# Kernel optimization log

Hardware: AMD Instinct MI355X
Metric: run time of the kernel (lower is better)

Reference implementation:

```python
import jax, jax.numpy as jnp
import numpy as np

EPS = 1e-12  # torch F.normalize eps

def _l2norm(x):
    n = jnp.linalg.norm(x, axis=-1, keepdims=True)
    return x / jnp.maximum(n, EPS)

def _encode(h, mask, W, b):
    # h: [B,S,H], mask: [B,S] int
    h = h * mask[..., None].astype(h.dtype)      # zero padded tokens
    pooled = h[:, 0]                             # pooling_type='cls'
    col = h[:, 1:] @ W + b                       # colbert_linear on tokens 1:
    return _l2norm(pooled), _l2norm(col)         # normalize=True


def setup_inputs() -> dict:
    key = jax.random.key(0)
    k1, k2, k3, k4, k5, k6 = jax.random.split(key, 6)
    Q, Sq, C, Sc, H, D = 64, 32, 256, 256, 768, 128
    return {
        "q_hidden": jax.random.normal(k1, (Q, Sq, H), jnp.float32),
        "c_hidden": jax.random.normal(k2, (C, Sc, H), jnp.float32),
        "W": jax.random.normal(k3, (H, D), jnp.float32) / np.sqrt(H).astype(np.float32),
        "b": jax.random.normal(k4, (D,), jnp.float32) * 0.01,
        "q_mask": jax.random.randint(k5, (Q, Sq), 0, 2, jnp.int32),
        "c_mask": jax.random.randint(k6, (C, Sc), 0, 2, jnp.int32),
    }


def reference(q_hidden, c_hidden, W, b, q_mask, c_mask):
    q_pooled, q_col = _encode(q_hidden, q_mask, W, b)   # q_col: [Q, Sq-1, D]
    c_pooled, c_col = _encode(c_hidden, c_mask, W, b)   # c_col: [C, Sc-1, D]
    # MaxSim late interaction (get_batch_colbert_sim)
    token_sim = jnp.einsum('qin,cjn->qicj', q_col, c_col)  # [Q, Sq-1, C, Sc-1]
    sim = token_sim.max(axis=-1)                           # max over doc tokens j
    denom = q_mask[:, 1:].sum(-1, keepdims=True).astype(sim.dtype)
    sim = sim.sum(axis=1) / denom                          # [Q, C]
    return sim, q_pooled, c_pooled
```

## Files before the change

kernel.cpp:

```cpp
#include <hip/hip_runtime.h>
#include <hip/hip_bf16.h>

#define QN 64
#define SQ 32
#define CN 256
#define SC 256
#define HD 768
#define DD 128

typedef __attribute__((ext_vector_type(8))) short short8;
typedef __attribute__((ext_vector_type(4))) float f32x4;

static __device__ __forceinline__ unsigned short f2bf(float x) {
  unsigned u = __float_as_uint(x);
  unsigned r = 0x7FFFu + ((u >> 16) & 1u);
  return (unsigned short)((u + r) >> 16);
}
static __device__ __forceinline__ unsigned pack2(float a, float b) {
  return (unsigned)f2bf(a) | ((unsigned)f2bf(b) << 16);
}

typedef const __attribute__((address_space(1))) unsigned int* as1_u32p;
typedef __attribute__((address_space(3))) unsigned int* as3_u32p;
static __device__ __forceinline__ void gl_lds16(const void* g, void* l) {
  __builtin_amdgcn_global_load_lds((as1_u32p)g, (as3_u32p)l, 16, 0, 0);
}

__global__ __launch_bounds__(256) void prep_kernel(
    const float* __restrict__ W,
    const float* __restrict__ qh, const int* __restrict__ qm,
    const float* __restrict__ ch, const int* __restrict__ cm,
    unsigned short* __restrict__ WtS,
    float* __restrict__ outq, float* __restrict__ outc,
    unsigned short* __restrict__ qcolP) {
  __shared__ float red[4];
  int bid = blockIdx.x, tid = threadIdx.x;

  if (bid < DD) {
    int d = bid;
    if (tid < 96) {
      int kc = tid;
      unsigned p[4];
#pragma unroll
      for (int e = 0; e < 4; ++e) {
        float a = W[(size_t)(kc * 8 + 2 * e) * DD + d];
        float b = W[(size_t)(kc * 8 + 2 * e + 1) * DD + d];
        p[e] = pack2(a, b);
      }
      int kcp = (kc & ~7) | ((kc & 7) ^ (d & 7));
      *(uint4*)&WtS[((size_t)d * 96 + kcp) * 8] = *(uint4*)p;
    }
    return;
  }

  int row = bid - DD;
  const float* src;
  float* dst;
  float m;
  if (row < QN) {
    src = qh + (size_t)row * SQ * HD;
    m = (float)qm[row * SQ];
    dst = outq + (size_t)row * HD;
  } else {
    int b = row - QN;
    src = ch + (size_t)b * SC * HD;
    m = (float)cm[b * SC];
    dst = outc + (size_t)b * HD;
  }
  float ss = 0.f;
  for (int k = tid; k < HD; k += 256) {
    float v = src[k] * m;
    ss += v * v;
  }
  int lane = tid & 63, wv = tid >> 6;
  for (int off = 32; off; off >>= 1) ss += __shfl_xor(ss, off);
  if (lane == 0) red[wv] = ss;
  __syncthreads();
  float tot = red[0] + red[1] + red[2] + red[3];
  float inv = 1.f / fmaxf(sqrtf(tot), 1e-12f);
  for (int k = tid; k < HD; k += 256) dst[k] = src[k] * m * inv;
  if (row < QN && tid < 64)
    ((unsigned*)(qcolP + ((size_t)row * 32 + 31) * DD))[tid] = 0u;
}

union ProjLDS {
  struct { float a[2][64 * 64]; unsigned short w[2][128 * 64]; } s;
  float cep[64 * 132];
};

__global__ __launch_bounds__(256, 2) void proj_kernel(
    const float* __restrict__ q_hidden, const float* __restrict__ c_hidden,
    const int* __restrict__ q_mask, const int* __restrict__ c_mask,
    const unsigned short* __restrict__ WtS, const float* __restrict__ bias,
    unsigned short* __restrict__ qcol, unsigned short* __restrict__ ccol) {
  __shared__ ProjLDS u;
  int bx = blockIdx.x;
  int isQ = (bx >= 1020) ? 1 : 0;
  int base = isQ ? (bx - 1020) : bx;
  int tid = threadIdx.x, lane = tid & 63, wv = tid >> 6;
  int lm = lane & 15, lq = lane >> 4;

  int ac = (tid & 8) | ((tid & 7) ^ ((tid >> 4) & 7));
  const float* aptr[4];
#pragma unroll
  for (int i = 0; i < 4; ++i) {
    int r = i * 16 + (tid >> 4);
    int g = base * 64 + r;
    const float* hp;
    if (isQ) {
      int qq = g / 31, t = g - qq * 31;
      hp = q_hidden + ((size_t)qq * SQ + t + 1) * HD;
    } else {
      int cb = g / 255, t = g - cb * 255;
      hp = c_hidden + ((size_t)cb * SC + t + 1) * HD;
    }
    aptr[i] = hp + ac * 4;
  }
  const unsigned short* wptr[4];
#pragma unroll
  for (int i = 0; i < 4; ++i) {
    int d = i * 32 + (tid >> 3);
    wptr[i] = WtS + ((size_t)d * 96 + (tid & 7)) * 8;
  }

  f32x4 acc[8];
#pragma unroll
  for (int j = 0; j < 8; ++j) acc[j] = (f32x4){0.f, 0.f, 0.f, 0.f};

#pragma unroll
  for (int i = 0; i < 4; ++i)
    gl_lds16(aptr[i], (char*)&u.s.a[0][0] + (size_t)(i * 256 + wv * 64) * 16);
#pragma unroll
  for (int i = 0; i < 4; ++i)
    gl_lds16(wptr[i], (char*)&u.s.w[0][0] + (size_t)(i * 256 + wv * 64) * 16);
  __syncthreads();

  for (int step = 0; step < 12; ++step) {
    int cur = step & 1;
    if (step < 11) {
      int nxt = cur ^ 1;
#pragma unroll
      for (int i = 0; i < 4; ++i)
        gl_lds16(aptr[i] + (step + 1) * 64,
                 (char*)&u.s.a[nxt][0] + (size_t)(i * 256 + wv * 64) * 16);
#pragma unroll
      for (int i = 0; i < 4; ++i)
        gl_lds16(wptr[i] + (step + 1) * 64,
                 (char*)&u.s.w[nxt][0] + (size_t)(i * 256 + wv * 64) * 16);
    }
#pragma unroll
    for (int w = 0; w < 2; ++w) {
      int rr = wv * 16 + lm;
      int x0 = (lq * 2) ^ (lm & 7);
      int x1 = (lq * 2 + 1) ^ (lm & 7);
      float4 a0 = *(const float4*)&u.s.a[cur][rr * 64 + w * 32 + x0 * 4];
      float4 a1 = *(const float4*)&u.s.a[cur][rr * 64 + w * 32 + x1 * 4];
      unsigned p[4];
      p[0] = pack2(a0.x, a0.y); p[1] = pack2(a0.z, a0.w);
      p[2] = pack2(a1.x, a1.y); p[3] = pack2(a1.z, a1.w);
      short8 afr = *(short8*)p;
#pragma unroll
      for (int nt = 0; nt < 8; ++nt) {
        int d = nt * 16 + lm;
        int pc = (w * 4 + lq) ^ (lm & 7);
        short8 bfr = *(const short8*)&u.s.w[cur][d * 64 + pc * 8];
        acc[nt] = __builtin_amdgcn_mfma_f32_16x16x32_bf16(afr, bfr, acc[nt], 0, 0, 0);
      }
    }
    __syncthreads();
  }

#pragma unroll
  for (int nt = 0; nt < 8; ++nt)
#pragma unroll
    for (int r = 0; r < 4; ++r) {
      int row = wv * 16 + lq * 4 + r;
      u.cep[row * 132 + nt * 16 + lm] = acc[nt][r];
    }
  __syncthreads();

  int tk = tid >> 2, qt = tid & 3;
  int g = base * 64 + tk;
  int qq, t;
  float fm;
  if (isQ) {
    qq = g / 31; t = g - qq * 31;
    fm = (float)q_mask[qq * SQ + t + 1];
  } else {
    qq = g / 255; t = g - qq * 255;
    fm = (float)c_mask[qq * SC + t + 1];
  }

  float v[32];
  float ss = 0.f;
#pragma unroll
  for (int j = 0; j < 8; ++j) {
    float4 cv = *(const float4*)&u.cep[tk * 132 + qt * 32 + j * 4];
    float4 bv = *(const float4*)&bias[qt * 32 + j * 4];
    v[4 * j + 0] = cv.x * fm + bv.x; v[4 * j + 1] = cv.y * fm + bv.y;
    v[4 * j + 2] = cv.z * fm + bv.z; v[4 * j + 3] = cv.w * fm + bv.w;
#pragma unroll
    for (int e = 0; e < 4; ++e) ss += v[4 * j + e] * v[4 * j + e];
  }
  ss += __shfl_xor(ss, 1);
  ss += __shfl_xor(ss, 2);
  float inv = 1.f / fmaxf(sqrtf(ss), 1e-12f);

  uint4 pk4[4];
#pragma unroll
  for (int j = 0; j < 4; ++j) {
    unsigned p[4];
#pragma unroll
    for (int e = 0; e < 4; ++e)
      p[e] = pack2(v[8 * j + 2 * e] * inv, v[8 * j + 2 * e + 1] * inv);
    pk4[j] = *(uint4*)p;
  }

  if (isQ) {
    uint4* dst = (uint4*)(qcol + ((size_t)qq * 32 + t) * DD + qt * 32);
#pragma unroll
    for (int j = 0; j < 4; ++j) dst[j] = pk4[j];
  } else {
    uint4* rowp = (uint4*)(ccol + ((size_t)qq * 256 + t) * DD);
#pragma unroll
    for (int j = 0; j < 4; ++j) {
      int kc = qt * 4 + j;
      int p = (kc & 8) | ((kc & 7) ^ (t & 7));
      rowp[p] = pk4[j];
    }
    if (t == 254) {
      uint4* rowp2 = rowp + 16;
#pragma unroll
      for (int j = 0; j < 4; ++j) {
        int kc = qt * 4 + j;
        int p = (kc & 8) | ((kc & 7) ^ 7);
        rowp2[p] = pk4[j];
      }
    }
  }
}

__global__ __launch_bounds__(256, 2) void sim_kernel(
    const unsigned short* __restrict__ qcolP,
    const unsigned short* __restrict__ ccol,
    const int* __restrict__ qmask,
    float* __restrict__ sim) {
  __shared__ unsigned short cbuf[2][128 * 128];
  int tid = threadIdx.x, lane = tid & 63, wv = tid >> 6;
  int lm = lane & 15, lq = lane >> 4;
  int qb = blockIdx.y * 16 + wv * 4;
  int c0 = blockIdx.x * 2;

  short8 af[4][2][4];
#pragma unroll
  for (int q2 = 0; q2 < 4; ++q2)
#pragma unroll
    for (int it = 0; it < 2; ++it)
#pragma unroll
      for (int kf = 0; kf < 4; ++kf)
        af[q2][it][kf] = *(const short8*)(qcolP +
            (((size_t)(qb + q2) * 32 + it * 16 + lm) * DD + kf * 32 + lq * 8));

  float dinv[4];
#pragma unroll
  for (int q2 = 0; q2 < 4; ++q2) {
    float v = (lane >= 1 && lane < 32) ? (float)qmask[(qb + q2) * SQ + lane] : 0.f;
    for (int off = 1; off < 64; off <<= 1) v += __shfl_xor(v, off);
    dinv[q2] = 1.f / v;
  }

  const unsigned short* csrc = ccol + (size_t)c0 * SC * DD;

#pragma unroll
  for (int i = 0; i < 8; ++i)
    gl_lds16(csrc + (size_t)(i * 256 + tid) * 8,
             (char*)&cbuf[0][0] + (size_t)(i * 256 + wv * 64) * 16);
  __syncthreads();

  float rmax[4][2];
  for (int ht = 0; ht < 4; ++ht) {
    int b = ht & 1;
    if (!(ht & 1)) {
#pragma unroll
      for (int q2 = 0; q2 < 4; ++q2) {
        rmax[q2][0] = -__builtin_inff();
        rmax[q2][1] = -__builtin_inff();
      }
    }
    if (ht < 3) {
      const unsigned short* s2 = csrc + (size_t)(ht + 1) * 16384;
#pragma unroll
      for (int i = 0; i < 8; ++i)
        gl_lds16(s2 + (size_t)(i * 256 + tid) * 8,
                 (char*)&cbuf[b ^ 1][0] + (size_t)(i * 256 + wv * 64) * 16);
    }

    for (int jt = 0; jt < 8; ++jt) {
      short8 cf[4];
#pragma unroll
      for (int kf = 0; kf < 4; ++kf) {
        int row = jt * 16 + lm;
        int kc = kf * 4 + lq;
        int p = (kc & 8) | ((kc & 7) ^ (row & 7));
        cf[kf] = *(const short8*)&cbuf[b][(size_t)(row * 16 + p) * 8];
      }
#pragma unroll
      for (int q2 = 0; q2 < 4; ++q2)
#pragma unroll
        for (int it = 0; it < 2; ++it) {
          f32x4 acc = (f32x4){0.f, 0.f, 0.f, 0.f};
#pragma unroll
          for (int kf = 0; kf < 4; ++kf)
            acc = __builtin_amdgcn_mfma_f32_16x16x32_bf16(cf[kf], af[q2][it][kf], acc, 0, 0, 0);
          float loc = fmaxf(fmaxf(acc[0], acc[1]), fmaxf(acc[2], acc[3]));
          rmax[q2][it] = fmaxf(rmax[q2][it], loc);
        }
    }

    if (ht & 1) {
      int c = c0 + (ht >> 1);
#pragma unroll
      for (int q2 = 0; q2 < 4; ++q2) {
        float m0 = rmax[q2][0], m1 = rmax[q2][1];
        m0 = fmaxf(m0, __shfl_xor(m0, 16)); m0 = fmaxf(m0, __shfl_xor(m0, 32));
        m1 = fmaxf(m1, __shfl_xor(m1, 16)); m1 = fmaxf(m1, __shfl_xor(m1, 32));
        float s = m0 + ((lm == 15) ? 0.f : m1);
        s += __shfl_xor(s, 1); s += __shfl_xor(s, 2);
        s += __shfl_xor(s, 4); s += __shfl_xor(s, 8);
        if (lane == 0) sim[(qb + q2) * CN + c] = s * dinv[q2];
      }
    }
    __syncthreads();
  }
}

extern "C" void kernel_launch(void* const* d_in, const int* in_sizes, int n_in,
                              void* d_out, int out_size, void* d_ws, size_t ws_size,
                              hipStream_t stream) {
  const float* q_hidden = (const float*)d_in[0];
  const float* c_hidden = (const float*)d_in[1];
  const float* W = (const float*)d_in[2];
  const float* bias = (const float*)d_in[3];
  const int* q_mask = (const int*)d_in[4];
  const int* c_mask = (const int*)d_in[5];

  float* out = (float*)d_out;
  float* sim = out;
  float* q_pooled = out + QN * CN;
  float* c_pooled = q_pooled + QN * HD;

  unsigned short* WtS   = (unsigned short*)d_ws;
  unsigned short* qcolP = (unsigned short*)((char*)d_ws + (256 << 10));
  unsigned short* ccol  = (unsigned short*)((char*)d_ws + (1 << 20));

  prep_kernel<<<DD + QN + CN, 256, 0, stream>>>(W, q_hidden, q_mask, c_hidden, c_mask,
                                                WtS, q_pooled, c_pooled, qcolP);
  proj_kernel<<<1051, 256, 0, stream>>>(q_hidden, c_hidden, q_mask, c_mask,
                                        WtS, bias, qcolP, ccol);
  sim_kernel<<<dim3(128, 4), 256, 0, stream>>>(qcolP, ccol, q_mask, sim);
}
```

Baseline: 361.3 us.

## Load projection activations directly to registers and double rows per block

```diff
diff --git a/kernel.cpp b/kernel.cpp
--- a/kernel.cpp
+++ b/kernel.cpp
@@ -84,7 +84,7 @@
 }
 
 union ProjLDS {
-  struct { float a[2][64 * 64]; unsigned short w[2][128 * 64]; } s;
+  unsigned short w[2][128 * 64];
   float cep[64 * 132];
 };
 
@@ -95,27 +95,27 @@
     unsigned short* __restrict__ qcol, unsigned short* __restrict__ ccol) {
   __shared__ ProjLDS u;
   int bx = blockIdx.x;
-  int isQ = (bx >= 1020) ? 1 : 0;
-  int base = isQ ? (bx - 1020) : bx;
+  int isQ = (bx >= 510) ? 1 : 0;
+  int base = isQ ? (bx - 510) : bx;
   int tid = threadIdx.x, lane = tid & 63, wv = tid >> 6;
   int lm = lane & 15, lq = lane >> 4;
 
-  int ac = (tid & 8) | ((tid & 7) ^ ((tid >> 4) & 7));
-  const float* aptr[4];
-#pragma unroll
-  for (int i = 0; i < 4; ++i) {
-    int r = i * 16 + (tid >> 4);
-    int g = base * 64 + r;
+  const float* abase[2];
+#pragma unroll
+  for (int mt = 0; mt < 2; ++mt) {
+    int g = base * 128 + wv * 32 + mt * 16 + lm;
     const float* hp;
     if (isQ) {
+      g = (g > 1983) ? 1983 : g;
       int qq = g / 31, t = g - qq * 31;
       hp = q_hidden + ((size_t)qq * SQ + t + 1) * HD;
     } else {
       int cb = g / 255, t = g - cb * 255;
       hp = c_hidden + ((size_t)cb * SC + t + 1) * HD;
     }
-    aptr[i] = hp + ac * 4;
-  }
+    abase[mt] = hp + lq * 8;
+  }
+
   const unsigned short* wptr[4];
 #pragma unroll
   for (int i = 0; i < 4; ++i) {
@@ -123,118 +123,151 @@
     wptr[i] = WtS + ((size_t)d * 96 + (tid & 7)) * 8;
   }
 
-  f32x4 acc[8];
-#pragma unroll
-  for (int j = 0; j < 8; ++j) acc[j] = (f32x4){0.f, 0.f, 0.f, 0.f};
-
+  f32x4 acc[2][8];
+#pragma unroll
+  for (int i = 0; i < 2; ++i)
+#pragma unroll
+    for (int j = 0; j < 8; ++j) acc[i][j] = (f32x4){0.f, 0.f, 0.f, 0.f};
+
+  float4 Pa[8], Pb[8];
+
+#pragma unroll
+  for (int w = 0; w < 2; ++w)
+#pragma unroll
+    for (int mt = 0; mt < 2; ++mt) {
+      Pa[w * 4 + mt * 2 + 0] = *(const float4*)(abase[mt] + w * 32);
+      Pa[w * 4 + mt * 2 + 1] = *(const float4*)(abase[mt] + w * 32 + 4);
+    }
 #pragma unroll
   for (int i = 0; i < 4; ++i)
-    gl_lds16(aptr[i], (char*)&u.s.a[0][0] + (size_t)(i * 256 + wv * 64) * 16);
-#pragma unroll
-  for (int i = 0; i < 4; ++i)
-    gl_lds16(wptr[i], (char*)&u.s.w[0][0] + (size_t)(i * 256 + wv * 64) * 16);
+    gl_lds16(wptr[i], (char*)&u.w[0][0] + (size_t)(i * 256 + wv * 64) * 16);
   __syncthreads();
 
-  for (int step = 0; step < 12; ++step) {
-    int cur = step & 1;
-    if (step < 11) {
-      int nxt = cur ^ 1;
-#pragma unroll
-      for (int i = 0; i < 4; ++i)
-        gl_lds16(aptr[i] + (step + 1) * 64,
-                 (char*)&u.s.a[nxt][0] + (size_t)(i * 256 + wv * 64) * 16);
-#pragma unroll
-      for (int i = 0; i < 4; ++i)
-        gl_lds16(wptr[i] + (step + 1) * 64,
-                 (char*)&u.s.w[nxt][0] + (size_t)(i * 256 + wv * 64) * 16);
-    }
-#pragma unroll
-    for (int w = 0; w < 2; ++w) {
-      int rr = wv * 16 + lm;
-      int x0 = (lq * 2) ^ (lm & 7);
-      int x1 = (lq * 2 + 1) ^ (lm & 7);
-      float4 a0 = *(const float4*)&u.s.a[cur][rr * 64 + w * 32 + x0 * 4];
-      float4 a1 = *(const float4*)&u.s.a[cur][rr * 64 + w * 32 + x1 * 4];
+#define PROJ_STEP(t, PC, PN, CB, NB, PREFETCH)                                 \
+  {                                                                            \
+    if (PREFETCH) {                                                            \
+      _Pragma("unroll")                                                        \
+      for (int w = 0; w < 2; ++w)                                              \
+        _Pragma("unroll")                                                      \
+        for (int mt = 0; mt < 2; ++mt) {                                       \
+          PN[w * 4 + mt * 2 + 0] =                                             \
+              *(const float4*)(abase[mt] + (t + 1) * 64 + w * 32);             \
+          PN[w * 4 + mt * 2 + 1] =                                             \
+              *(const float4*)(abase[mt] + (t + 1) * 64 + w * 32 + 4);         \
+        }                                                                      \
+      _Pragma("unroll")                                                        \
+      for (int i = 0; i < 4; ++i)                                              \
+        gl_lds16(wptr[i] + (t + 1) * 64,                                       \
+                 (char*)&u.w[NB][0] + (size_t)(i * 256 + wv * 64) * 16);       \
+    }                                                                          \
+    _Pragma("unroll")                                                          \
+    for (int w = 0; w < 2; ++w) {                                              \
+      short8 afr[2];                                                           \
+      _Pragma("unroll")                                                        \
+      for (int mt = 0; mt < 2; ++mt) {                                         \
+        float4 a0 = PC[w * 4 + mt * 2], a1 = PC[w * 4 + mt * 2 + 1];           \
+        unsigned pk[4];                                                        \
+        pk[0] = pack2(a0.x, a0.y); pk[1] = pack2(a0.z, a0.w);                  \
+        pk[2] = pack2(a1.x, a1.y); pk[3] = pack2(a1.z, a1.w);                  \
+        afr[mt] = *(short8*)pk;                                                \
+      }                                                                        \
+      _Pragma("unroll")                                                        \
+      for (int nt = 0; nt < 8; ++nt) {                                         \
+        int d = nt * 16 + lm;                                                  \
+        int pc = (w * 4 + lq) ^ (lm & 7);                                      \
+        short8 bfr = *(const short8*)&u.w[CB][d * 64 + pc * 8];                \
+        acc[0][nt] = __builtin_amdgcn_mfma_f32_16x16x32_bf16(afr[0], bfr,      \
+                                                             acc[0][nt], 0, 0, 0); \
+        acc[1][nt] = __builtin_amdgcn_mfma_f32_16x16x32_bf16(afr[1], bfr,      \
+                                                             acc[1][nt], 0, 0, 0); \
+      }                                                                        \
+    }                                                                          \
+    __syncthreads();                                                           \
+  }
+
+#pragma unroll
+  for (int s = 0; s < 12; s += 2) {
+    PROJ_STEP(s, Pa, Pb, 0, 1, 1);
+    PROJ_STEP(s + 1, Pb, Pa, 1, 0, (s + 1 < 11));
+  }
+#undef PROJ_STEP
+
+  int tk = tid >> 2, qt = tid & 3;
+#pragma unroll
+  for (int h = 0; h < 2; ++h) {
+    __syncthreads();
+    if ((wv >> 1) == h) {
+#pragma unroll
+      for (int mt = 0; mt < 2; ++mt)
+#pragma unroll
+        for (int nt = 0; nt < 8; ++nt)
+#pragma unroll
+          for (int r = 0; r < 4; ++r) {
+            int row = (wv & 1) * 32 + mt * 16 + lq * 4 + r;
+            u.cep[row * 132 + nt * 16 + lm] = acc[mt][nt][r];
+          }
+    }
+    __syncthreads();
+
+    int g = base * 128 + h * 64 + tk;
+    int qq, t, valid = 1;
+    float fm;
+    if (isQ) {
+      if (g > 1983) { valid = 0; g = 1983; }
+      qq = g / 31; t = g - qq * 31;
+      fm = (float)q_mask[qq * SQ + t + 1];
+    } else {
+      qq = g / 255; t = g - qq * 255;
+      fm = (float)c_mask[qq * SC + t + 1];
+    }
+
+    float v[32];
+    float ss = 0.f;
+#pragma unroll
+    for (int j = 0; j < 8; ++j) {
+      float4 cv = *(const float4*)&u.cep[tk * 132 + qt * 32 + j * 4];
+      float4 bv = *(const float4*)&bias[qt * 32 + j * 4];
+      v[4 * j + 0] = cv.x * fm + bv.x; v[4 * j + 1] = cv.y * fm + bv.y;
+      v[4 * j + 2] = cv.z * fm + bv.z; v[4 * j + 3] = cv.w * fm + bv.w;
+#pragma unroll
+      for (int e = 0; e < 4; ++e) ss += v[4 * j + e] * v[4 * j + e];
+    }
+    ss += __shfl_xor(ss, 1);
+    ss += __shfl_xor(ss, 2);
+    float inv = 1.f / fmaxf(sqrtf(ss), 1e-12f);
+
+    uint4 pk4[4];
+#pragma unroll
+    for (int j = 0; j < 4; ++j) {
       unsigned p[4];
-      p[0] = pack2(a0.x, a0.y); p[1] = pack2(a0.z, a0.w);
-      p[2] = pack2(a1.x, a1.y); p[3] = pack2(a1.z, a1.w);
-      short8 afr = *(short8*)p;
-#pragma unroll
-      for (int nt = 0; nt < 8; ++nt) {
-        int d = nt * 16 + lm;
-        int pc = (w * 4 + lq) ^ (lm & 7);
-        short8 bfr = *(const short8*)&u.s.w[cur][d * 64 + pc * 8];
-        acc[nt] = __builtin_amdgcn_mfma_f32_16x16x32_bf16(afr, bfr, acc[nt], 0, 0, 0);
-      }
-    }
-    __syncthreads();
-  }
-
-#pragma unroll
-  for (int nt = 0; nt < 8; ++nt)
-#pragma unroll
-    for (int r = 0; r < 4; ++r) {
-      int row = wv * 16 + lq * 4 + r;
-      u.cep[row * 132 + nt * 16 + lm] = acc[nt][r];
-    }
-  __syncthreads();
-
-  int tk = tid >> 2, qt = tid & 3;
-  int g = base * 64 + tk;
-  int qq, t;
-  float fm;
-  if (isQ) {
-    qq = g / 31; t = g - qq * 31;
-    fm = (float)q_mask[qq * SQ + t + 1];
-  } else {
-    qq = g / 255; t = g - qq * 255;
-    fm = (float)c_mask[qq * SC + t + 1];
-  }
-
-  float v[32];
-  float ss = 0.f;
-#pragma unroll
-  for (int j = 0; j < 8; ++j) {
-    float4 cv = *(const float4*)&u.cep[tk * 132 + qt * 32 + j * 4];
-    float4 bv = *(const float4*)&bias[qt * 32 + j * 4];
-    v[4 * j + 0] = cv.x * fm + bv.x; v[4 * j + 1] = cv.y * fm + bv.y;
-    v[4 * j + 2] = cv.z * fm + bv.z; v[4 * j + 3] = cv.w * fm + bv.w;
-#pragma unroll
-    for (int e = 0; e < 4; ++e) ss += v[4 * j + e] * v[4 * j + e];
-  }
-  ss += __shfl_xor(ss, 1);
-  ss += __shfl_xor(ss, 2);
-  float inv = 1.f / fmaxf(sqrtf(ss), 1e-12f);
-
-  uint4 pk4[4];
-#pragma unroll
-  for (int j = 0; j < 4; ++j) {
-    unsigned p[4];
-#pragma unroll
-    for (int e = 0; e < 4; ++e)
-      p[e] = pack2(v[8 * j + 2 * e] * inv, v[8 * j + 2 * e + 1] * inv);
-    pk4[j] = *(uint4*)p;
-  }
-
-  if (isQ) {
-    uint4* dst = (uint4*)(qcol + ((size_t)qq * 32 + t) * DD + qt * 32);
-#pragma unroll
-    for (int j = 0; j < 4; ++j) dst[j] = pk4[j];
-  } else {
-    uint4* rowp = (uint4*)(ccol + ((size_t)qq * 256 + t) * DD);
-#pragma unroll
-    for (int j = 0; j < 4; ++j) {
-      int kc = qt * 4 + j;
-      int p = (kc & 8) | ((kc & 7) ^ (t & 7));
-      rowp[p] = pk4[j];
-    }
-    if (t == 254) {
-      uint4* rowp2 = rowp + 16;
+#pragma unroll
+      for (int e = 0; e < 4; ++e)
+        p[e] = pack2(v[8 * j + 2 * e] * inv, v[8 * j + 2 * e + 1] * inv);
+      pk4[j] = *(uint4*)p;
+    }
+
+    if (isQ) {
+      if (valid) {
+        uint4* dst = (uint4*)(qcol + ((size_t)qq * 32 + t) * DD + qt * 32);
+#pragma unroll
+        for (int j = 0; j < 4; ++j) dst[j] = pk4[j];
+      }
+    } else {
+      uint4* rowp = (uint4*)(ccol + ((size_t)qq * 256 + t) * DD);
 #pragma unroll
       for (int j = 0; j < 4; ++j) {
         int kc = qt * 4 + j;
-        int p = (kc & 8) | ((kc & 7) ^ 7);
-        rowp2[p] = pk4[j];
+        int p = (kc & 8) | ((kc & 7) ^ (t & 7));
+        rowp[p] = pk4[j];
+      }
+      if (t == 254) {
+        uint4* rowp2 = rowp + 16;
+#pragma unroll
+        for (int j = 0; j < 4; ++j) {
+          int kc = qt * 4 + j;
+          int p = (kc & 8) | ((kc & 7) ^ 7);
+          rowp2[p] = pk4[j];
+        }
       }
     }
   }
@@ -355,7 +388,7 @@
 
   prep_kernel<<<DD + QN + CN, 256, 0, stream>>>(W, q_hidden, q_mask, c_hidden, c_mask,
                                                 WtS, q_pooled, c_pooled, qcolP);
-  proj_kernel<<<1051, 256, 0, stream>>>(q_hidden, c_hidden, q_mask, c_mask,
-                                        WtS, bias, qcolP, ccol);
+  proj_kernel<<<526, 256, 0, stream>>>(q_hidden, c_hidden, q_mask, c_mask,
+                                       WtS, bias, qcolP, ccol);
   sim_kernel<<<dim3(128, 4), 256, 0, stream>>>(qcolP, ccol, q_mask, sim);
 }
```

Measured after the change: 373.6 us. 1.03x slower.

## Preload full bf16 A tile into LDS and halve projection row tile

Applied to the files above, without the earlier changes.

```diff
diff --git a/kernel.cpp b/kernel.cpp
--- a/kernel.cpp
+++ b/kernel.cpp
@@ -83,9 +83,9 @@
     ((unsigned*)(qcolP + ((size_t)row * 32 + 31) * DD))[tid] = 0u;
 }
 
-union ProjLDS {
-  struct { float a[2][64 * 64]; unsigned short w[2][128 * 64]; } s;
-  float cep[64 * 132];
+union ProjWLDS {
+  unsigned short w[2][128 * 64];
+  float cep[32 * 132];
 };
 
 __global__ __launch_bounds__(256, 2) void proj_kernel(
@@ -93,29 +93,36 @@
     const int* __restrict__ q_mask, const int* __restrict__ c_mask,
     const unsigned short* __restrict__ WtS, const float* __restrict__ bias,
     unsigned short* __restrict__ qcol, unsigned short* __restrict__ ccol) {
-  __shared__ ProjLDS u;
+  __shared__ unsigned short Alds[32 * 768];
+  __shared__ ProjWLDS u;
   int bx = blockIdx.x;
-  int isQ = (bx >= 1020) ? 1 : 0;
-  int base = isQ ? (bx - 1020) : bx;
+  int isQ = (bx >= 2040) ? 1 : 0;
+  int base = isQ ? (bx - 2040) : bx;
   int tid = threadIdx.x, lane = tid & 63, wv = tid >> 6;
   int lm = lane & 15, lq = lane >> 4;
-
-  int ac = (tid & 8) | ((tid & 7) ^ ((tid >> 4) & 7));
-  const float* aptr[4];
-#pragma unroll
-  for (int i = 0; i < 4; ++i) {
-    int r = i * 16 + (tid >> 4);
-    int g = base * 64 + r;
+  int wi = wv & 1;
+  int wj = wv >> 1;
+
+  const float* asrc[12];
+  unsigned aoff[12];
+#pragma unroll
+  for (int i = 0; i < 12; ++i) {
+    unsigned j = i * 256 + tid;
+    unsigned row = j / 96, c = j - row * 96;
+    unsigned g = base * 32 + row;
     const float* hp;
     if (isQ) {
-      int qq = g / 31, t = g - qq * 31;
+      unsigned qq = g / 31, t = g - qq * 31;
       hp = q_hidden + ((size_t)qq * SQ + t + 1) * HD;
     } else {
-      int cb = g / 255, t = g - cb * 255;
+      unsigned cb = g / 255, t = g - cb * 255;
       hp = c_hidden + ((size_t)cb * SC + t + 1) * HD;
     }
-    aptr[i] = hp + ac * 4;
-  }
+    asrc[i] = hp + c * 8;
+    unsigned cp = (c & ~7u) | ((c & 7u) ^ (row & 7u));
+    aoff[i] = row * 768 + cp * 8;
+  }
+
   const unsigned short* wptr[4];
 #pragma unroll
   for (int i = 0; i < 4; ++i) {
@@ -123,64 +130,65 @@
     wptr[i] = WtS + ((size_t)d * 96 + (tid & 7)) * 8;
   }
 
-  f32x4 acc[8];
-#pragma unroll
-  for (int j = 0; j < 8; ++j) acc[j] = (f32x4){0.f, 0.f, 0.f, 0.f};
-
+  float4 av[12][2];
+#pragma unroll
+  for (int i = 0; i < 12; ++i) {
+    av[i][0] = *(const float4*)(asrc[i]);
+    av[i][1] = *(const float4*)(asrc[i] + 4);
+  }
 #pragma unroll
   for (int i = 0; i < 4; ++i)
-    gl_lds16(aptr[i], (char*)&u.s.a[0][0] + (size_t)(i * 256 + wv * 64) * 16);
-#pragma unroll
-  for (int i = 0; i < 4; ++i)
-    gl_lds16(wptr[i], (char*)&u.s.w[0][0] + (size_t)(i * 256 + wv * 64) * 16);
+    gl_lds16(wptr[i], (char*)&u.w[0][0] + (size_t)(i * 256 + wv * 64) * 16);
+
+#pragma unroll
+  for (int i = 0; i < 12; ++i) {
+    unsigned pk[4];
+    pk[0] = pack2(av[i][0].x, av[i][0].y);
+    pk[1] = pack2(av[i][0].z, av[i][0].w);
+    pk[2] = pack2(av[i][1].x, av[i][1].y);
+    pk[3] = pack2(av[i][1].z, av[i][1].w);
+    *(uint4*)&Alds[aoff[i]] = *(uint4*)pk;
+  }
+
+  f32x4 acc[4];
+#pragma unroll
+  for (int n = 0; n < 4; ++n) acc[n] = (f32x4){0.f, 0.f, 0.f, 0.f};
+
   __syncthreads();
 
-  for (int step = 0; step < 12; ++step) {
-    int cur = step & 1;
-    if (step < 11) {
-      int nxt = cur ^ 1;
+  int arow = 16 * wi + lm;
+  for (int t = 0; t < 12; ++t) {
+    int cb_ = t & 1;
+    if (t < 11) {
 #pragma unroll
       for (int i = 0; i < 4; ++i)
-        gl_lds16(aptr[i] + (step + 1) * 64,
-                 (char*)&u.s.a[nxt][0] + (size_t)(i * 256 + wv * 64) * 16);
-#pragma unroll
-      for (int i = 0; i < 4; ++i)
-        gl_lds16(wptr[i] + (step + 1) * 64,
-                 (char*)&u.s.w[nxt][0] + (size_t)(i * 256 + wv * 64) * 16);
+        gl_lds16(wptr[i] + (t + 1) * 64,
+                 (char*)&u.w[cb_ ^ 1][0] + (size_t)(i * 256 + wv * 64) * 16);
     }
 #pragma unroll
     for (int w = 0; w < 2; ++w) {
-      int rr = wv * 16 + lm;
-      int x0 = (lq * 2) ^ (lm & 7);
-      int x1 = (lq * 2 + 1) ^ (lm & 7);
-      float4 a0 = *(const float4*)&u.s.a[cur][rr * 64 + w * 32 + x0 * 4];
-      float4 a1 = *(const float4*)&u.s.a[cur][rr * 64 + w * 32 + x1 * 4];
-      unsigned p[4];
-      p[0] = pack2(a0.x, a0.y); p[1] = pack2(a0.z, a0.w);
-      p[2] = pack2(a1.x, a1.y); p[3] = pack2(a1.z, a1.w);
-      short8 afr = *(short8*)p;
-#pragma unroll
-      for (int nt = 0; nt < 8; ++nt) {
-        int d = nt * 16 + lm;
+      int coct = t * 8 + ((w * 4 + lq) ^ (lm & 7));
+      short8 afr = *(const short8*)&Alds[arow * 768 + coct * 8];
+#pragma unroll
+      for (int n = 0; n < 4; ++n) {
+        int d = (wj * 4 + n) * 16 + lm;
         int pc = (w * 4 + lq) ^ (lm & 7);
-        short8 bfr = *(const short8*)&u.s.w[cur][d * 64 + pc * 8];
-        acc[nt] = __builtin_amdgcn_mfma_f32_16x16x32_bf16(afr, bfr, acc[nt], 0, 0, 0);
+        short8 bfr = *(const short8*)&u.w[cb_][d * 64 + pc * 8];
+        acc[n] = __builtin_amdgcn_mfma_f32_16x16x32_bf16(afr, bfr, acc[n], 0, 0, 0);
       }
     }
     __syncthreads();
   }
 
 #pragma unroll
-  for (int nt = 0; nt < 8; ++nt)
-#pragma unroll
-    for (int r = 0; r < 4; ++r) {
-      int row = wv * 16 + lq * 4 + r;
-      u.cep[row * 132 + nt * 16 + lm] = acc[nt][r];
-    }
+  for (int n = 0; n < 4; ++n)
+#pragma unroll
+    for (int r = 0; r < 4; ++r)
+      u.cep[(16 * wi + lq * 4 + r) * 132 + wj * 64 + n * 16 + lm] = acc[n][r];
   __syncthreads();
 
-  int tk = tid >> 2, qt = tid & 3;
-  int g = base * 64 + tk;
+  int tk = tid >> 3, qt = tid & 7;
+  int g = base * 32 + tk;
   int qq, t;
   float fm;
   if (isQ) {
@@ -191,12 +199,12 @@
     fm = (float)c_mask[qq * SC + t + 1];
   }
 
-  float v[32];
+  float v[16];
   float ss = 0.f;
 #pragma unroll
-  for (int j = 0; j < 8; ++j) {
-    float4 cv = *(const float4*)&u.cep[tk * 132 + qt * 32 + j * 4];
-    float4 bv = *(const float4*)&bias[qt * 32 + j * 4];
+  for (int j = 0; j < 4; ++j) {
+    float4 cv = *(const float4*)&u.cep[tk * 132 + qt * 16 + j * 4];
+    float4 bv = *(const float4*)&bias[qt * 16 + j * 4];
     v[4 * j + 0] = cv.x * fm + bv.x; v[4 * j + 1] = cv.y * fm + bv.y;
     v[4 * j + 2] = cv.z * fm + bv.z; v[4 * j + 3] = cv.w * fm + bv.w;
 #pragma unroll
@@ -204,11 +212,12 @@
   }
   ss += __shfl_xor(ss, 1);
   ss += __shfl_xor(ss, 2);
+  ss += __shfl_xor(ss, 4);
   float inv = 1.f / fmaxf(sqrtf(ss), 1e-12f);
 
-  uint4 pk4[4];
-#pragma unroll
-  for (int j = 0; j < 4; ++j) {
+  uint4 pk4[2];
+#pragma unroll
+  for (int j = 0; j < 2; ++j) {
     unsigned p[4];
 #pragma unroll
     for (int e = 0; e < 4; ++e)
@@ -217,22 +226,22 @@
   }
 
   if (isQ) {
-    uint4* dst = (uint4*)(qcol + ((size_t)qq * 32 + t) * DD + qt * 32);
-#pragma unroll
-    for (int j = 0; j < 4; ++j) dst[j] = pk4[j];
+    uint4* dst = (uint4*)(qcol + ((size_t)qq * 32 + t) * DD);
+#pragma unroll
+    for (int j = 0; j < 2; ++j) dst[qt * 2 + j] = pk4[j];
   } else {
     uint4* rowp = (uint4*)(ccol + ((size_t)qq * 256 + t) * DD);
 #pragma unroll
-    for (int j = 0; j < 4; ++j) {
-      int kc = qt * 4 + j;
+    for (int j = 0; j < 2; ++j) {
+      int kc = qt * 2 + j;
       int p = (kc & 8) | ((kc & 7) ^ (t & 7));
       rowp[p] = pk4[j];
     }
     if (t == 254) {
       uint4* rowp2 = rowp + 16;
 #pragma unroll
-      for (int j = 0; j < 4; ++j) {
-        int kc = qt * 4 + j;
+      for (int j = 0; j < 2; ++j) {
+        int kc = qt * 2 + j;
         int p = (kc & 8) | ((kc & 7) ^ 7);
         rowp2[p] = pk4[j];
       }
@@ -355,7 +364,7 @@
 
   prep_kernel<<<DD + QN + CN, 256, 0, stream>>>(W, q_hidden, q_mask, c_hidden, c_mask,
                                                 WtS, q_pooled, c_pooled, qcolP);
-  proj_kernel<<<1051, 256, 0, stream>>>(q_hidden, c_hidden, q_mask, c_mask,
+  proj_kernel<<<2102, 256, 0, stream>>>(q_hidden, c_hidden, q_mask, c_mask,
                                         WtS, bias, qcolP, ccol);
   sim_kernel<<<dim3(128, 4), 256, 0, stream>>>(qcolP, ccol, q_mask, sim);
 }
```

Result: slower. 379.5 us (+5.0%).
